# Optimization experiments

Hardware: AMD Instinct MI355X
Metric: run time of the kernel (lower is better)

The kernel has to match this reference:

```python
import jax, jax.numpy as jnp
import numpy as np

HID = 128  # args['hidden_size']


def preprocess_adj(A):
    # A: [B, N, N] -> D^{-1/2} (A + I) D^{-1/2}
    N = A.shape[1]
    A_hat = A + jnp.eye(N, dtype=A.dtype)
    d = jnp.sum(A_hat, axis=2)                     # [B, N]
    d_safe = jnp.where(d > 0, d, 1.0)
    d_inv = jnp.where(d > 0, d_safe ** -0.5, 0.0)  # inf -> 0, as in torch code
    return d_inv[:, :, None] * A_hat * d_inv[:, None, :]


def lstm(x, w_ih, w_hh, b_ih, b_hh):
    # x: [B, T, H]; PyTorch gate order i, f, g, o; zero init state
    B = x.shape[0]
    H = w_hh.shape[1]
    def step(carry, xt):
        h, c = carry
        z = xt @ w_ih.T + b_ih + h @ w_hh.T + b_hh
        i, f, g, o = jnp.split(z, 4, axis=-1)
        c = jax.nn.sigmoid(f) * c + jax.nn.sigmoid(i) * jnp.tanh(g)
        h = jax.nn.sigmoid(o) * jnp.tanh(c)
        return (h, c), h
    h0 = jnp.zeros((B, H), x.dtype)
    c0 = jnp.zeros((B, H), x.dtype)
    _, hs = jax.lax.scan(step, (h0, c0), jnp.swapaxes(x, 0, 1))
    return jnp.swapaxes(hs, 0, 1)  # [B, T, H]


def gcn_dynamic_forward(x, A_norm, conv_w, conv_b, w_ih, w_hh, b_ih, b_hh):
    # x: [B, N, HID] with N >= HID: take last HID rows as dynamic-filter input
    df_in = x[:, x.shape[1] - HID:, :]              # [B, HID, HID]
    dyn = jax.lax.conv_general_dilated(
        df_in, conv_w, window_strides=(1,), padding=[(1, 1)],
        dimension_numbers=('NCH', 'OIH', 'NCH')) + conv_b[None, :, None]
    lw = lstm(dyn, w_ih, w_hh, b_ih, b_hh)          # [B, HID, HID]
    agg = jnp.matmul(A_norm, x)                     # [B, N, HID]
    out = jax.nn.sigmoid(jnp.matmul(agg, lw))       # output activation (1-layer GCN)
    return out                                       # dropout is identity in eval


def setup_inputs() -> dict:
    key = jax.random.key(0)
    ks = jax.random.split(key, 8)
    B, N = 4, 4096
    node_embedding = jax.random.normal(ks[0], (B, N, HID), dtype=jnp.float32)
    # sparse symmetric-ish 0/1 adjacency, avg degree ~ N*0.01
    adjacency_matrix = (jax.random.uniform(ks[1], (B, N, N)) < 0.01).astype(jnp.float32)
    s = 0.05
    conv_w = jax.random.normal(ks[2], (HID, HID, 3), dtype=jnp.float32) * s
    conv_b = jax.random.normal(ks[3], (HID,), dtype=jnp.float32) * s
    w_ih = jax.random.normal(ks[4], (4 * HID, HID), dtype=jnp.float32) * s
    w_hh = jax.random.normal(ks[5], (4 * HID, HID), dtype=jnp.float32) * s
    b_ih = jax.random.normal(ks[6], (4 * HID,), dtype=jnp.float32) * s
    b_hh = jax.random.normal(ks[7], (4 * HID,), dtype=jnp.float32) * s
    return {"node_embedding": node_embedding, "adjacency_matrix": adjacency_matrix,
            "conv_w": conv_w, "conv_b": conv_b,
            "w_ih": w_ih, "w_hh": w_hh, "b_ih": b_ih, "b_hh": b_hh}


def reference(node_embedding, adjacency_matrix, conv_w, conv_b, w_ih, w_hh, b_ih, b_hh):
    A_norm = preprocess_adj(adjacency_matrix)
    return gcn_dynamic_forward(node_embedding, A_norm, conv_w, conv_b, w_ih, w_hh, b_ih, b_hh)
```

## Files before the change

### kernel.cpp

```cpp
#include <hip/hip_runtime.h>
#include <math.h>

#define N_NODES 4096
#define HIDN 128
#define MAXNZ 128

typedef float v4f __attribute__((ext_vector_type(4)));
typedef _Float16 h2 __attribute__((ext_vector_type(2)));
typedef _Float16 h8 __attribute__((ext_vector_type(8)));

__device__ __forceinline__ float fsig(float x) { return 1.0f / (1.0f + __expf(-x)); }
__device__ __forceinline__ float ftanh_(float x) { return 1.0f - 2.0f / (__expf(2.0f * x) + 1.0f); }

__global__ __launch_bounds__(512) void k1_conv_ascan(
        const float* __restrict__ x, const float* __restrict__ conv_w,
        const float* __restrict__ conv_b, const float* __restrict__ w_ih,
        const float* __restrict__ b_ih, const float* __restrict__ b_hh,
        float* __restrict__ z3,
        const float* __restrict__ A, float* __restrict__ d_inv,
        int* __restrict__ cnt, int* __restrict__ idx) {
    __shared__ __align__(16) float dyn_lds[4][HIDN];
    __shared__ int sidx[8][MAXNZ];
    if (blockIdx.x < 128) {
        const int cb = blockIdx.x;
        const int b = cb >> 5;
        const int t0 = (cb & 31) * 4;
        const int tsub = threadIdx.x >> 7;
        const int h = threadIdx.x & 127;
        const int t = t0 + tsub;
        {
            const float* xb = x + ((size_t)b * N_NODES + (N_NODES - HIDN)) * HIDN;
            const float* w = conv_w + (size_t)t * HIDN * 3;
            float a0 = conv_b[t], a1 = 0.0f, a2 = 0.0f, a3 = 0.0f;
            #pragma unroll 4
            for (int i = 0; i < HIDN; i += 4) {
                const float* xr0 = xb + (size_t)i * HIDN;
                #pragma unroll
                for (int s = 0; s < 4; ++s) {
                    const float* xr = xr0 + s * HIDN;
                    float w0 = w[(i + s) * 3 + 0], w1 = w[(i + s) * 3 + 1], w2 = w[(i + s) * 3 + 2];
                    float left  = (h > 0)   ? xr[h - 1] : 0.0f;
                    float mid   = xr[h];
                    float right = (h < 127) ? xr[h + 1] : 0.0f;
                    if (s == 0)      a0 += left * w0 + mid * w1 + right * w2;
                    else if (s == 1) a1 += left * w0 + mid * w1 + right * w2;
                    else if (s == 2) a2 += left * w0 + mid * w1 + right * w2;
                    else             a3 += left * w0 + mid * w1 + right * w2;
                }
            }
            dyn_lds[tsub][h] = (a0 + a1) + (a2 + a3);
        }
        __syncthreads();
        const int u = threadIdx.x;
        const int qg = u >> 7;
        const int m  = u & 127;
        const float4* wr = (const float4*)(w_ih + (size_t)u * HIDN);
        float bias = b_ih[u] + b_hh[u];
        float acc0 = bias, acc1 = bias, acc2 = bias, acc3 = bias;
        #pragma unroll
        for (int half = 0; half < 2; ++half) {
            float4 wv[16];
            #pragma unroll
            for (int j = 0; j < 16; ++j) wv[j] = wr[half * 16 + j];
            const float4* d0 = (const float4*)dyn_lds[0] + half * 16;
            const float4* d1 = (const float4*)dyn_lds[1] + half * 16;
            const float4* d2 = (const float4*)dyn_lds[2] + half * 16;
            const float4* d3 = (const float4*)dyn_lds[3] + half * 16;
            #pragma unroll
            for (int j = 0; j < 16; ++j) {
                float4 wj = wv[j];
                float4 v0 = d0[j], v1 = d1[j], v2 = d2[j], v3 = d3[j];
                acc0 += wj.x * v0.x + wj.y * v0.y + wj.z * v0.z + wj.w * v0.w;
                acc1 += wj.x * v1.x + wj.y * v1.y + wj.z * v1.z + wj.w * v1.w;
                acc2 += wj.x * v2.x + wj.y * v2.y + wj.z * v2.z + wj.w * v2.w;
                acc3 += wj.x * v3.x + wj.y * v3.y + wj.z * v3.z + wj.w * v3.w;
            }
        }
        float* zb = z3 + (size_t)b * HIDN * HIDN * 4;
        zb[((size_t)(t0 + 0) * 128 + m) * 4 + qg] = acc0;
        zb[((size_t)(t0 + 1) * 128 + m) * 4 + qg] = acc1;
        zb[((size_t)(t0 + 2) * 128 + m) * 4 + qg] = acc2;
        zb[((size_t)(t0 + 3) * 128 + m) * 4 + qg] = acc3;
    } else {
        const int wid = threadIdx.x >> 6;
        const int lane = threadIdx.x & 63;
        const int r = (blockIdx.x - 128) * 8 + wid;
        const v4f* row = (const v4f*)(A + (size_t)r * N_NODES);
        const unsigned long long below = (1ull << lane) - 1ull;
        int cbase = 0;
        v4f cur[4], nxt[4];
        #pragma unroll
        for (int j = 0; j < 4; ++j) cur[j] = row[j * 64 + lane];
#define PROC1(c, col)                                                         \
        {                                                                     \
            bool nz = ((c) != 0.0f);                                          \
            unsigned long long mm = __ballot(nz);                             \
            if (mm) {                                                         \
                if (nz) {                                                     \
                    int p_ = cbase + __popcll(mm & below);                    \
                    if (p_ < MAXNZ) sidx[wid][p_] = (col);                    \
                }                                                             \
                cbase += __popcll(mm);                                        \
            }                                                                 \
        }
        #pragma unroll
        for (int g = 0; g < 4; ++g) {
            if (g < 3) {
                #pragma unroll
                for (int j = 0; j < 4; ++j) nxt[j] = row[(g + 1) * 256 + j * 64 + lane];
            }
            #pragma unroll
            for (int j = 0; j < 4; ++j) {
                int col0 = ((g * 4 + j) * 64 + lane) * 4;
                PROC1(cur[j].x, col0 + 0);
                PROC1(cur[j].y, col0 + 1);
                PROC1(cur[j].z, col0 + 2);
                PROC1(cur[j].w, col0 + 3);
            }
            #pragma unroll
            for (int j = 0; j < 4; ++j) cur[j] = nxt[j];
        }
#undef PROC1
        int cnt_r = (cbase < MAXNZ) ? cbase : MAXNZ;
        for (int k = lane; k < cnt_r; k += 64)
            idx[r * MAXNZ + k] = sidx[wid][k];
        if (lane == 0) {
            cnt[r] = cnt_r;
            d_inv[r] = rsqrtf((float)(cbase + 1));
        }
    }
}

__global__ __launch_bounds__(512, 2) void k2_lstm_gather(
        const float* __restrict__ z3, const float* __restrict__ w_hh,
        float* __restrict__ lw,
        const float* __restrict__ x, const float* __restrict__ d_inv,
        const int* __restrict__ cnt, const int* __restrict__ idx,
        float* __restrict__ agg) {
    __shared__ __align__(16) float4 zl[16 * 128];
    __shared__ __align__(16) _Float16 hbuf[2][HIDN];
    if (blockIdx.x < 4) {
        const int b = blockIdx.x;
        const int t = threadIdx.x;
        const int m = t >> 2;
        const int q = t & 3;
        h2 w2[4][16];
        #pragma unroll
        for (int g = 0; g < 4; ++g) {
            const float4* wr = (const float4*)(w_hh + ((size_t)(g * HIDN + m)) * HIDN + q * 32);
            #pragma unroll
            for (int j4 = 0; j4 < 8; ++j4) {
                float4 wv = wr[j4];
                w2[g][2 * j4 + 0] = h2{(_Float16)wv.x, (_Float16)wv.y};
                w2[g][2 * j4 + 1] = h2{(_Float16)wv.z, (_Float16)wv.w};
            }
        }
        float c = 0.0f;
        if (t < 64) ((h2*)hbuf[0])[t] = h2{(_Float16)0.0f, (_Float16)0.0f};
        const float4* zsrc = (const float4*)z3 + (size_t)b * 16384;
        float* lwb = lw + (size_t)b * HIDN * HIDN + m;
        float hist[4];
        for (int ch = 0; ch < 8; ++ch) {
            const float4* src = zsrc + ch * 2048;
            #pragma unroll
            for (int k = 0; k < 4; ++k)
                zl[t + 512 * k] = src[t + 512 * k];
            __syncthreads();
            #pragma unroll
            for (int si = 0; si < 16; ++si) {
                const int s = ch * 16 + si;
                const h8* hp = ((const h8*)hbuf[s & 1]) + q * 4;
                h8 H0 = hp[0], H1 = hp[1], H2 = hp[2], H3 = hp[3];
                h2 hh[16];
                #pragma unroll
                for (int j = 0; j < 4; ++j) {
                    hh[j]      = ((const h2*)&H0)[j];
                    hh[4 + j]  = ((const h2*)&H1)[j];
                    hh[8 + j]  = ((const h2*)&H2)[j];
                    hh[12 + j] = ((const h2*)&H3)[j];
                }
                float4 zv = zl[si * 128 + m];
                float a0 = 0.f, a1 = 0.f, a2 = 0.f, a3 = 0.f;
                #pragma unroll
                for (int j = 0; j < 16; ++j) {
                    a0 = __builtin_amdgcn_fdot2(w2[0][j], hh[j], a0, false);
                    a1 = __builtin_amdgcn_fdot2(w2[1][j], hh[j], a1, false);
                    a2 = __builtin_amdgcn_fdot2(w2[2][j], hh[j], a2, false);
                    a3 = __builtin_amdgcn_fdot2(w2[3][j], hh[j], a3, false);
                }
                a0 += __shfl_xor(a0, 1); a0 += __shfl_xor(a0, 2);
                a1 += __shfl_xor(a1, 1); a1 += __shfl_xor(a1, 2);
                a2 += __shfl_xor(a2, 1); a2 += __shfl_xor(a2, 2);
                a3 += __shfl_xor(a3, 1); a3 += __shfl_xor(a3, 2);
                float zi = a0 + zv.x;
                float zf = a1 + zv.y;
                float zg = a2 + zv.z;
                float zo = a3 + zv.w;
                float ig = fsig(zi);
                float fg = fsig(zf);
                float gg = ftanh_(zg);
                float og = fsig(zo);
                c = fg * c + ig * gg;
                float hn = og * ftanh_(c);
                if (q == (si & 3)) hist[si >> 2] = hn;
                if (q == 0) hbuf[(s + 1) & 1][m] = (_Float16)hn;
                __syncthreads();
            }
            #pragma unroll
            for (int j = 0; j < 4; ++j)
                lwb[(size_t)(ch * 16 + q + 4 * j) * HIDN] = hist[j];
        }
    } else {
        const int gIdx = blockIdx.x - 4;
        const int b = (gIdx & 7) >> 1;
        const int o = ((gIdx >> 3) << 1) | (gIdx & 1);
        const int wid = threadIdx.x >> 6;
        const int lane = threadIdx.x & 63;
        float* dl = (float*)zl;
        {
            const float4* dsrc = (const float4*)(d_inv + (b << 12));
            float4* ddst = (float4*)dl;
            ddst[threadIdx.x] = dsrc[threadIdx.x];
            ddst[threadIdx.x + 512] = dsrc[threadIdx.x + 512];
        }
        __syncthreads();
        const int i = o * 8 + wid;
        const int r = (b << 12) + i;
        const float2* xb = (const float2*)(x + (size_t)b * N_NODES * HIDN);
        const int* irow = idx + r * MAXNZ;
        const int n = cnt[r];
        float ax = 0.0f, ay = 0.0f;
        int k = 0;
        for (; k + 8 <= n; k += 8) {
            int4 j0 = *(const int4*)&irow[k];
            int4 j1 = *(const int4*)&irow[k + 4];
            float2 v0 = xb[(size_t)j0.x * 64 + lane];
            float2 v1 = xb[(size_t)j0.y * 64 + lane];
            float2 v2 = xb[(size_t)j0.z * 64 + lane];
            float2 v3 = xb[(size_t)j0.w * 64 + lane];
            float2 v4 = xb[(size_t)j1.x * 64 + lane];
            float2 v5 = xb[(size_t)j1.y * 64 + lane];
            float2 v6 = xb[(size_t)j1.z * 64 + lane];
            float2 v7 = xb[(size_t)j1.w * 64 + lane];
            float d0 = dl[j0.x], d1 = dl[j0.y], d2 = dl[j0.z], d3 = dl[j0.w];
            float d4 = dl[j1.x], d5 = dl[j1.y], d6 = dl[j1.z], d7 = dl[j1.w];
            ax += d0 * v0.x + d1 * v1.x + d2 * v2.x + d3 * v3.x
                + d4 * v4.x + d5 * v5.x + d6 * v6.x + d7 * v7.x;
            ay += d0 * v0.y + d1 * v1.y + d2 * v2.y + d3 * v3.y
                + d4 * v4.y + d5 * v5.y + d6 * v6.y + d7 * v7.y;
        }
        for (; k < n; ++k) {
            int j = irow[k];
            float dj = dl[j];
            float2 v = xb[(size_t)j * 64 + lane];
            ax += dj * v.x;
            ay += dj * v.y;
        }
        float di = dl[i];
        float2 vi = xb[(size_t)i * 64 + lane];
        float2 o2;
        o2.x = di * (ax + di * vi.x);
        o2.y = di * (ay + di * vi.y);
        ((float2*)(agg + (size_t)r * HIDN))[lane] = o2;
    }
}

__global__ __launch_bounds__(256) void k_outmm(
        const float* __restrict__ agg, const float* __restrict__ lw,
        float* __restrict__ out) {
    __shared__ __align__(16) float lw_lds[HIDN * HIDN];
    const int i0 = blockIdx.x * 64;
    const int b = i0 >> 12;
    const float4* lwg = (const float4*)(lw + (size_t)b * HIDN * HIDN);
    float4* lds4 = (float4*)lw_lds;
    for (int v = threadIdx.x; v < HIDN * HIDN / 4; v += 256) lds4[v] = lwg[v];
    __syncthreads();
    const int r0 = i0 + (threadIdx.x >> 3) * 2;
    const int u0 = (threadIdx.x & 7) * 16;
    const float4* a4 = (const float4*)agg;
    float4 acc[2][4];
    #pragma unroll
    for (int rr = 0; rr < 2; ++rr)
        #pragma unroll
        for (int cc = 0; cc < 4; ++cc) acc[rr][cc] = make_float4(0.f, 0.f, 0.f, 0.f);
    for (int f4 = 0; f4 < 32; ++f4) {
        float4 a0 = a4[(size_t)r0 * 32 + f4];
        float4 a1 = a4[(size_t)(r0 + 1) * 32 + f4];
        #pragma unroll
        for (int ff = 0; ff < 4; ++ff) {
            float af0 = (ff == 0) ? a0.x : (ff == 1) ? a0.y : (ff == 2) ? a0.z : a0.w;
            float af1 = (ff == 0) ? a1.x : (ff == 1) ? a1.y : (ff == 2) ? a1.z : a1.w;
            int f = f4 * 4 + ff;
            const float4* wrow = (const float4*)(lw_lds + f * HIDN + u0);
            #pragma unroll
            for (int cc = 0; cc < 4; ++cc) {
                float4 wv = wrow[cc];
                acc[0][cc].x += af0 * wv.x; acc[0][cc].y += af0 * wv.y;
                acc[0][cc].z += af0 * wv.z; acc[0][cc].w += af0 * wv.w;
                acc[1][cc].x += af1 * wv.x; acc[1][cc].y += af1 * wv.y;
                acc[1][cc].z += af1 * wv.z; acc[1][cc].w += af1 * wv.w;
            }
        }
    }
    #pragma unroll
    for (int rr = 0; rr < 2; ++rr) {
        #pragma unroll
        for (int cc = 0; cc < 4; ++cc) {
            float4 ov;
            ov.x = fsig(acc[rr][cc].x);
            ov.y = fsig(acc[rr][cc].y);
            ov.z = fsig(acc[rr][cc].z);
            ov.w = fsig(acc[rr][cc].w);
            *(float4*)(out + (size_t)(r0 + rr) * HIDN + u0 + cc * 4) = ov;
        }
    }
}

extern "C" void kernel_launch(void* const* d_in, const int* in_sizes, int n_in,
                              void* d_out, int out_size, void* d_ws, size_t ws_size,
                              hipStream_t stream) {
    const float* x      = (const float*)d_in[0];
    const float* A      = (const float*)d_in[1];
    const float* conv_w = (const float*)d_in[2];
    const float* conv_b = (const float*)d_in[3];
    const float* w_ih   = (const float*)d_in[4];
    const float* w_hh   = (const float*)d_in[5];
    const float* b_ih   = (const float*)d_in[6];
    const float* b_hh   = (const float*)d_in[7];
    float* out = (float*)d_out;

    char* ws = (char*)d_ws;
    float* d_inv = (float*)ws;
    int*   cnt   = (int*)(ws + 65536);
    int*   idx   = (int*)(ws + 131072);
    float* z3    = (float*)(ws + 131072 + 8388608);
    float* lw    = (float*)(ws + 131072 + 8388608 + 1048576);
    float* agg   = (float*)(ws + 131072 + 8388608 + 1048576 + 262144);

    hipLaunchKernelGGL(k1_conv_ascan, dim3(2176), dim3(512), 0, stream,
                       x, conv_w, conv_b, w_ih, b_ih, b_hh, z3, A, d_inv, cnt, idx);
    hipLaunchKernelGGL(k2_lstm_gather, dim3(2052), dim3(512), 0, stream,
                       z3, w_hh, lw, x, d_inv, cnt, idx, agg);
    hipLaunchKernelGGL(k_outmm, dim3(256), dim3(256), 0, stream, agg, lw, out);
}
```

Before: 500.7 us.

## Overlap LSTM recurrence with adjacency scan and split gather into own kernel

Moves the adjacency-row scan from the conv kernel into the LSTM kernel so the serial 4-block LSTM recurrence runs alongside the memory-bound A scan rather than alongside the gather. The conv/z kernel and the gather now run as separate launches, giving four kernels in total. The output matmul is retiled to 512 threads over 32 rows per block with one row per thread. The LSTM inner loop also selects h pairs inline instead of staging them in an array. The extra launch and changed overlap could lengthen the critical path if the LSTM is the long pole.

```diff
diff --git a/kernel.cpp b/kernel.cpp
--- a/kernel.cpp
+++ b/kernel.cpp
@@ -12,133 +12,81 @@
 __device__ __forceinline__ float fsig(float x) { return 1.0f / (1.0f + __expf(-x)); }
 __device__ __forceinline__ float ftanh_(float x) { return 1.0f - 2.0f / (__expf(2.0f * x) + 1.0f); }
 
-__global__ __launch_bounds__(512) void k1_conv_ascan(
+__global__ __launch_bounds__(512) void k_convz(
         const float* __restrict__ x, const float* __restrict__ conv_w,
         const float* __restrict__ conv_b, const float* __restrict__ w_ih,
         const float* __restrict__ b_ih, const float* __restrict__ b_hh,
-        float* __restrict__ z3,
+        float* __restrict__ z3) {
+    const int cb = blockIdx.x;
+    const int b = cb >> 5;
+    const int t0 = (cb & 31) * 4;
+    const int tsub = threadIdx.x >> 7;
+    const int h = threadIdx.x & 127;
+    const int t = t0 + tsub;
+    __shared__ __align__(16) float dyn_lds[4][HIDN];
+    {
+        const float* xb = x + ((size_t)b * N_NODES + (N_NODES - HIDN)) * HIDN;
+        const float* w = conv_w + (size_t)t * HIDN * 3;
+        float a0 = conv_b[t], a1 = 0.0f, a2 = 0.0f, a3 = 0.0f;
+        #pragma unroll 4
+        for (int i = 0; i < HIDN; i += 4) {
+            const float* xr0 = xb + (size_t)i * HIDN;
+            #pragma unroll
+            for (int s = 0; s < 4; ++s) {
+                const float* xr = xr0 + s * HIDN;
+                float w0 = w[(i + s) * 3 + 0], w1 = w[(i + s) * 3 + 1], w2 = w[(i + s) * 3 + 2];
+                float left  = (h > 0)   ? xr[h - 1] : 0.0f;
+                float mid   = xr[h];
+                float right = (h < 127) ? xr[h + 1] : 0.0f;
+                if (s == 0)      a0 += left * w0 + mid * w1 + right * w2;
+                else if (s == 1) a1 += left * w0 + mid * w1 + right * w2;
+                else if (s == 2) a2 += left * w0 + mid * w1 + right * w2;
+                else             a3 += left * w0 + mid * w1 + right * w2;
+            }
+        }
+        dyn_lds[tsub][h] = (a0 + a1) + (a2 + a3);
+    }
+    __syncthreads();
+    const int u = threadIdx.x;
+    const int qg = u >> 7;
+    const int m  = u & 127;
+    const float4* wr = (const float4*)(w_ih + (size_t)u * HIDN);
+    float bias = b_ih[u] + b_hh[u];
+    float acc0 = bias, acc1 = bias, acc2 = bias, acc3 = bias;
+    #pragma unroll
+    for (int half = 0; half < 2; ++half) {
+        float4 wv[16];
+        #pragma unroll
+        for (int j = 0; j < 16; ++j) wv[j] = wr[half * 16 + j];
+        const float4* d0 = (const float4*)dyn_lds[0] + half * 16;
+        const float4* d1 = (const float4*)dyn_lds[1] + half * 16;
+        const float4* d2 = (const float4*)dyn_lds[2] + half * 16;
+        const float4* d3 = (const float4*)dyn_lds[3] + half * 16;
+        #pragma unroll
+        for (int j = 0; j < 16; ++j) {
+            float4 wj = wv[j];
+            float4 v0 = d0[j], v1 = d1[j], v2 = d2[j], v3 = d3[j];
+            acc0 += wj.x * v0.x + wj.y * v0.y + wj.z * v0.z + wj.w * v0.w;
+            acc1 += wj.x * v1.x + wj.y * v1.y + wj.z * v1.z + wj.w * v1.w;
+            acc2 += wj.x * v2.x + wj.y * v2.y + wj.z * v2.z + wj.w * v2.w;
+            acc3 += wj.x * v3.x + wj.y * v3.y + wj.z * v3.z + wj.w * v3.w;
+        }
+    }
+    float* zb = z3 + (size_t)b * HIDN * HIDN * 4;
+    zb[((size_t)(t0 + 0) * 128 + m) * 4 + qg] = acc0;
+    zb[((size_t)(t0 + 1) * 128 + m) * 4 + qg] = acc1;
+    zb[((size_t)(t0 + 2) * 128 + m) * 4 + qg] = acc2;
+    zb[((size_t)(t0 + 3) * 128 + m) * 4 + qg] = acc3;
+}
+
+__global__ __launch_bounds__(512, 2) void k_lstm_scan(
+        const float* __restrict__ z3, const float* __restrict__ w_hh,
+        float* __restrict__ lw,
         const float* __restrict__ A, float* __restrict__ d_inv,
         int* __restrict__ cnt, int* __restrict__ idx) {
-    __shared__ __align__(16) float dyn_lds[4][HIDN];
-    __shared__ int sidx[8][MAXNZ];
-    if (blockIdx.x < 128) {
-        const int cb = blockIdx.x;
-        const int b = cb >> 5;
-        const int t0 = (cb & 31) * 4;
-        const int tsub = threadIdx.x >> 7;
-        const int h = threadIdx.x & 127;
-        const int t = t0 + tsub;
-        {
-            const float* xb = x + ((size_t)b * N_NODES + (N_NODES - HIDN)) * HIDN;
-            const float* w = conv_w + (size_t)t * HIDN * 3;
-            float a0 = conv_b[t], a1 = 0.0f, a2 = 0.0f, a3 = 0.0f;
-            #pragma unroll 4
-            for (int i = 0; i < HIDN; i += 4) {
-                const float* xr0 = xb + (size_t)i * HIDN;
-                #pragma unroll
-                for (int s = 0; s < 4; ++s) {
-                    const float* xr = xr0 + s * HIDN;
-                    float w0 = w[(i + s) * 3 + 0], w1 = w[(i + s) * 3 + 1], w2 = w[(i + s) * 3 + 2];
-                    float left  = (h > 0)   ? xr[h - 1] : 0.0f;
-                    float mid   = xr[h];
-                    float right = (h < 127) ? xr[h + 1] : 0.0f;
-                    if (s == 0)      a0 += left * w0 + mid * w1 + right * w2;
-                    else if (s == 1) a1 += left * w0 + mid * w1 + right * w2;
-                    else if (s == 2) a2 += left * w0 + mid * w1 + right * w2;
-                    else             a3 += left * w0 + mid * w1 + right * w2;
-                }
-            }
-            dyn_lds[tsub][h] = (a0 + a1) + (a2 + a3);
-        }
-        __syncthreads();
-        const int u = threadIdx.x;
-        const int qg = u >> 7;
-        const int m  = u & 127;
-        const float4* wr = (const float4*)(w_ih + (size_t)u * HIDN);
-        float bias = b_ih[u] + b_hh[u];
-        float acc0 = bias, acc1 = bias, acc2 = bias, acc3 = bias;
-        #pragma unroll
-        for (int half = 0; half < 2; ++half) {
-            float4 wv[16];
-            #pragma unroll
-            for (int j = 0; j < 16; ++j) wv[j] = wr[half * 16 + j];
-            const float4* d0 = (const float4*)dyn_lds[0] + half * 16;
-            const float4* d1 = (const float4*)dyn_lds[1] + half * 16;
-            const float4* d2 = (const float4*)dyn_lds[2] + half * 16;
-            const float4* d3 = (const float4*)dyn_lds[3] + half * 16;
-            #pragma unroll
-            for (int j = 0; j < 16; ++j) {
-                float4 wj = wv[j];
-                float4 v0 = d0[j], v1 = d1[j], v2 = d2[j], v3 = d3[j];
-                acc0 += wj.x * v0.x + wj.y * v0.y + wj.z * v0.z + wj.w * v0.w;
-                acc1 += wj.x * v1.x + wj.y * v1.y + wj.z * v1.z + wj.w * v1.w;
-                acc2 += wj.x * v2.x + wj.y * v2.y + wj.z * v2.z + wj.w * v2.w;
-                acc3 += wj.x * v3.x + wj.y * v3.y + wj.z * v3.z + wj.w * v3.w;
-            }
-        }
-        float* zb = z3 + (size_t)b * HIDN * HIDN * 4;
-        zb[((size_t)(t0 + 0) * 128 + m) * 4 + qg] = acc0;
-        zb[((size_t)(t0 + 1) * 128 + m) * 4 + qg] = acc1;
-        zb[((size_t)(t0 + 2) * 128 + m) * 4 + qg] = acc2;
-        zb[((size_t)(t0 + 3) * 128 + m) * 4 + qg] = acc3;
-    } else {
-        const int wid = threadIdx.x >> 6;
-        const int lane = threadIdx.x & 63;
-        const int r = (blockIdx.x - 128) * 8 + wid;
-        const v4f* row = (const v4f*)(A + (size_t)r * N_NODES);
-        const unsigned long long below = (1ull << lane) - 1ull;
-        int cbase = 0;
-        v4f cur[4], nxt[4];
-        #pragma unroll
-        for (int j = 0; j < 4; ++j) cur[j] = row[j * 64 + lane];
-#define PROC1(c, col)                                                         \
-        {                                                                     \
-            bool nz = ((c) != 0.0f);                                          \
-            unsigned long long mm = __ballot(nz);                             \
-            if (mm) {                                                         \
-                if (nz) {                                                     \
-                    int p_ = cbase + __popcll(mm & below);                    \
-                    if (p_ < MAXNZ) sidx[wid][p_] = (col);                    \
-                }                                                             \
-                cbase += __popcll(mm);                                        \
-            }                                                                 \
-        }
-        #pragma unroll
-        for (int g = 0; g < 4; ++g) {
-            if (g < 3) {
-                #pragma unroll
-                for (int j = 0; j < 4; ++j) nxt[j] = row[(g + 1) * 256 + j * 64 + lane];
-            }
-            #pragma unroll
-            for (int j = 0; j < 4; ++j) {
-                int col0 = ((g * 4 + j) * 64 + lane) * 4;
-                PROC1(cur[j].x, col0 + 0);
-                PROC1(cur[j].y, col0 + 1);
-                PROC1(cur[j].z, col0 + 2);
-                PROC1(cur[j].w, col0 + 3);
-            }
-            #pragma unroll
-            for (int j = 0; j < 4; ++j) cur[j] = nxt[j];
-        }
-#undef PROC1
-        int cnt_r = (cbase < MAXNZ) ? cbase : MAXNZ;
-        for (int k = lane; k < cnt_r; k += 64)
-            idx[r * MAXNZ + k] = sidx[wid][k];
-        if (lane == 0) {
-            cnt[r] = cnt_r;
-            d_inv[r] = rsqrtf((float)(cbase + 1));
-        }
-    }
-}
-
-__global__ __launch_bounds__(512, 2) void k2_lstm_gather(
-        const float* __restrict__ z3, const float* __restrict__ w_hh,
-        float* __restrict__ lw,
-        const float* __restrict__ x, const float* __restrict__ d_inv,
-        const int* __restrict__ cnt, const int* __restrict__ idx,
-        float* __restrict__ agg) {
     __shared__ __align__(16) float4 zl[16 * 128];
     __shared__ __align__(16) _Float16 hbuf[2][HIDN];
+    __shared__ int sidx[8][MAXNZ];
     if (blockIdx.x < 4) {
         const int b = blockIdx.x;
         const int t = threadIdx.x;
@@ -171,22 +119,18 @@
                 const int s = ch * 16 + si;
                 const h8* hp = ((const h8*)hbuf[s & 1]) + q * 4;
                 h8 H0 = hp[0], H1 = hp[1], H2 = hp[2], H3 = hp[3];
-                h2 hh[16];
-                #pragma unroll
-                for (int j = 0; j < 4; ++j) {
-                    hh[j]      = ((const h2*)&H0)[j];
-                    hh[4 + j]  = ((const h2*)&H1)[j];
-                    hh[8 + j]  = ((const h2*)&H2)[j];
-                    hh[12 + j] = ((const h2*)&H3)[j];
-                }
                 float4 zv = zl[si * 128 + m];
                 float a0 = 0.f, a1 = 0.f, a2 = 0.f, a3 = 0.f;
                 #pragma unroll
                 for (int j = 0; j < 16; ++j) {
-                    a0 = __builtin_amdgcn_fdot2(w2[0][j], hh[j], a0, false);
-                    a1 = __builtin_amdgcn_fdot2(w2[1][j], hh[j], a1, false);
-                    a2 = __builtin_amdgcn_fdot2(w2[2][j], hh[j], a2, false);
-                    a3 = __builtin_amdgcn_fdot2(w2[3][j], hh[j], a3, false);
+                    h2 hj = (j < 4)  ? ((const h2*)&H0)[j]
+                          : (j < 8)  ? ((const h2*)&H1)[j - 4]
+                          : (j < 12) ? ((const h2*)&H2)[j - 8]
+                                     : ((const h2*)&H3)[j - 12];
+                    a0 = __builtin_amdgcn_fdot2(w2[0][j], hj, a0, false);
+                    a1 = __builtin_amdgcn_fdot2(w2[1][j], hj, a1, false);
+                    a2 = __builtin_amdgcn_fdot2(w2[2][j], hj, a2, false);
+                    a3 = __builtin_amdgcn_fdot2(w2[3][j], hj, a3, false);
                 }
                 a0 += __shfl_xor(a0, 1); a0 += __shfl_xor(a0, 2);
                 a1 += __shfl_xor(a1, 1); a1 += __shfl_xor(a1, 2);
@@ -211,108 +155,150 @@
                 lwb[(size_t)(ch * 16 + q + 4 * j) * HIDN] = hist[j];
         }
     } else {
-        const int gIdx = blockIdx.x - 4;
-        const int b = (gIdx & 7) >> 1;
-        const int o = ((gIdx >> 3) << 1) | (gIdx & 1);
         const int wid = threadIdx.x >> 6;
         const int lane = threadIdx.x & 63;
-        float* dl = (float*)zl;
-        {
-            const float4* dsrc = (const float4*)(d_inv + (b << 12));
-            float4* ddst = (float4*)dl;
-            ddst[threadIdx.x] = dsrc[threadIdx.x];
-            ddst[threadIdx.x + 512] = dsrc[threadIdx.x + 512];
-        }
-        __syncthreads();
-        const int i = o * 8 + wid;
-        const int r = (b << 12) + i;
-        const float2* xb = (const float2*)(x + (size_t)b * N_NODES * HIDN);
-        const int* irow = idx + r * MAXNZ;
-        const int n = cnt[r];
-        float ax = 0.0f, ay = 0.0f;
-        int k = 0;
-        for (; k + 8 <= n; k += 8) {
-            int4 j0 = *(const int4*)&irow[k];
-            int4 j1 = *(const int4*)&irow[k + 4];
-            float2 v0 = xb[(size_t)j0.x * 64 + lane];
-            float2 v1 = xb[(size_t)j0.y * 64 + lane];
-            float2 v2 = xb[(size_t)j0.z * 64 + lane];
-            float2 v3 = xb[(size_t)j0.w * 64 + lane];
-            float2 v4 = xb[(size_t)j1.x * 64 + lane];
-            float2 v5 = xb[(size_t)j1.y * 64 + lane];
-            float2 v6 = xb[(size_t)j1.z * 64 + lane];
-            float2 v7 = xb[(size_t)j1.w * 64 + lane];
-            float d0 = dl[j0.x], d1 = dl[j0.y], d2 = dl[j0.z], d3 = dl[j0.w];
-            float d4 = dl[j1.x], d5 = dl[j1.y], d6 = dl[j1.z], d7 = dl[j1.w];
-            ax += d0 * v0.x + d1 * v1.x + d2 * v2.x + d3 * v3.x
-                + d4 * v4.x + d5 * v5.x + d6 * v6.x + d7 * v7.x;
-            ay += d0 * v0.y + d1 * v1.y + d2 * v2.y + d3 * v3.y
-                + d4 * v4.y + d5 * v5.y + d6 * v6.y + d7 * v7.y;
-        }
-        for (; k < n; ++k) {
-            int j = irow[k];
-            float dj = dl[j];
-            float2 v = xb[(size_t)j * 64 + lane];
-            ax += dj * v.x;
-            ay += dj * v.y;
-        }
-        float di = dl[i];
-        float2 vi = xb[(size_t)i * 64 + lane];
-        float2 o2;
-        o2.x = di * (ax + di * vi.x);
-        o2.y = di * (ay + di * vi.y);
-        ((float2*)(agg + (size_t)r * HIDN))[lane] = o2;
-    }
-}
-
-__global__ __launch_bounds__(256) void k_outmm(
+        const int r = (blockIdx.x - 4) * 8 + wid;
+        const v4f* row = (const v4f*)(A + (size_t)r * N_NODES);
+        const unsigned long long below = (1ull << lane) - 1ull;
+        int cbase = 0;
+        v4f cur[4], nxt[4];
+        #pragma unroll
+        for (int j = 0; j < 4; ++j) cur[j] = row[j * 64 + lane];
+#define PROC1(c, col)                                                         \
+        {                                                                     \
+            bool nz = ((c) != 0.0f);                                          \
+            unsigned long long mm = __ballot(nz);                             \
+            if (mm) {                                                         \
+                if (nz) {                                                     \
+                    int p_ = cbase + __popcll(mm & below);                    \
+                    if (p_ < MAXNZ) sidx[wid][p_] = (col);                    \
+                }                                                             \
+                cbase += __popcll(mm);                                        \
+            }                                                                 \
+        }
+        #pragma unroll
+        for (int g = 0; g < 4; ++g) {
+            if (g < 3) {
+                #pragma unroll
+                for (int j = 0; j < 4; ++j) nxt[j] = row[(g + 1) * 256 + j * 64 + lane];
+            }
+            #pragma unroll
+            for (int j = 0; j < 4; ++j) {
+                int col0 = ((g * 4 + j) * 64 + lane) * 4;
+                PROC1(cur[j].x, col0 + 0);
+                PROC1(cur[j].y, col0 + 1);
+                PROC1(cur[j].z, col0 + 2);
+                PROC1(cur[j].w, col0 + 3);
+            }
+            #pragma unroll
+            for (int j = 0; j < 4; ++j) cur[j] = nxt[j];
+        }
+#undef PROC1
+        int cnt_r = (cbase < MAXNZ) ? cbase : MAXNZ;
+        for (int k = lane; k < cnt_r; k += 64)
+            idx[r * MAXNZ + k] = sidx[wid][k];
+        if (lane == 0) {
+            cnt[r] = cnt_r;
+            d_inv[r] = rsqrtf((float)(cbase + 1));
+        }
+    }
+}
+
+__global__ __launch_bounds__(512) void k_gather(
+        const float* __restrict__ x, const float* __restrict__ d_inv,
+        const int* __restrict__ cnt, const int* __restrict__ idx,
+        float* __restrict__ agg) {
+    const int gIdx = blockIdx.x;
+    const int b = (gIdx & 7) >> 1;
+    const int o = ((gIdx >> 3) << 1) | (gIdx & 1);
+    const int wid = threadIdx.x >> 6;
+    const int lane = threadIdx.x & 63;
+    __shared__ __align__(16) float dl[N_NODES];
+    {
+        const float4* dsrc = (const float4*)(d_inv + (b << 12));
+        float4* ddst = (float4*)dl;
+        ddst[threadIdx.x] = dsrc[threadIdx.x];
+        ddst[threadIdx.x + 512] = dsrc[threadIdx.x + 512];
+    }
+    __syncthreads();
+    const int i = o * 8 + wid;
+    const int r = (b << 12) + i;
+    const float2* xb = (const float2*)(x + (size_t)b * N_NODES * HIDN);
+    const int* irow = idx + r * MAXNZ;
+    const int n = cnt[r];
+    float ax = 0.0f, ay = 0.0f;
+    int k = 0;
+    for (; k + 8 <= n; k += 8) {
+        int4 j0 = *(const int4*)&irow[k];
+        int4 j1 = *(const int4*)&irow[k + 4];
+        float2 v0 = xb[(size_t)j0.x * 64 + lane];
+        float2 v1 = xb[(size_t)j0.y * 64 + lane];
+        float2 v2 = xb[(size_t)j0.z * 64 + lane];
+        float2 v3 = xb[(size_t)j0.w * 64 + lane];
+        float2 v4 = xb[(size_t)j1.x * 64 + lane];
+        float2 v5 = xb[(size_t)j1.y * 64 + lane];
+        float2 v6 = xb[(size_t)j1.z * 64 + lane];
+        float2 v7 = xb[(size_t)j1.w * 64 + lane];
+        float d0 = dl[j0.x], d1 = dl[j0.y], d2 = dl[j0.z], d3 = dl[j0.w];
+        float d4 = dl[j1.x], d5 = dl[j1.y], d6 = dl[j1.z], d7 = dl[j1.w];
+        ax += d0 * v0.x + d1 * v1.x + d2 * v2.x + d3 * v3.x
+            + d4 * v4.x + d5 * v5.x + d6 * v6.x + d7 * v7.x;
+        ay += d0 * v0.y + d1 * v1.y + d2 * v2.y + d3 * v3.y
+            + d4 * v4.y + d5 * v5.y + d6 * v6.y + d7 * v7.y;
+    }
+    for (; k < n; ++k) {
+        int j = irow[k];
+        float dj = dl[j];
+        float2 v = xb[(size_t)j * 64 + lane];
+        ax += dj * v.x;
+        ay += dj * v.y;
+    }
+    float di = dl[i];
+    float2 vi = xb[(size_t)i * 64 + lane];
+    float2 o2;
+    o2.x = di * (ax + di * vi.x);
+    o2.y = di * (ay + di * vi.y);
+    ((float2*)(agg + (size_t)r * HIDN))[lane] = o2;
+}
+
+__global__ __launch_bounds__(512) void k_outmm(
         const float* __restrict__ agg, const float* __restrict__ lw,
         float* __restrict__ out) {
     __shared__ __align__(16) float lw_lds[HIDN * HIDN];
-    const int i0 = blockIdx.x * 64;
+    const int i0 = blockIdx.x * 32;
     const int b = i0 >> 12;
     const float4* lwg = (const float4*)(lw + (size_t)b * HIDN * HIDN);
     float4* lds4 = (float4*)lw_lds;
-    for (int v = threadIdx.x; v < HIDN * HIDN / 4; v += 256) lds4[v] = lwg[v];
+    for (int v = threadIdx.x; v < HIDN * HIDN / 4; v += 512) lds4[v] = lwg[v];
     __syncthreads();
-    const int r0 = i0 + (threadIdx.x >> 3) * 2;
-    const int u0 = (threadIdx.x & 7) * 16;
+    const int r0 = i0 + (threadIdx.x >> 4);
+    const int u0 = (threadIdx.x & 15) * 4;
     const float4* a4 = (const float4*)agg;
-    float4 acc[2][4];
-    #pragma unroll
-    for (int rr = 0; rr < 2; ++rr)
-        #pragma unroll
-        for (int cc = 0; cc < 4; ++cc) acc[rr][cc] = make_float4(0.f, 0.f, 0.f, 0.f);
+    float4 acc[2];
+    acc[0] = make_float4(0.f, 0.f, 0.f, 0.f);
+    acc[1] = make_float4(0.f, 0.f, 0.f, 0.f);
     for (int f4 = 0; f4 < 32; ++f4) {
         float4 a0 = a4[(size_t)r0 * 32 + f4];
-        float4 a1 = a4[(size_t)(r0 + 1) * 32 + f4];
         #pragma unroll
         for (int ff = 0; ff < 4; ++ff) {
             float af0 = (ff == 0) ? a0.x : (ff == 1) ? a0.y : (ff == 2) ? a0.z : a0.w;
-            float af1 = (ff == 0) ? a1.x : (ff == 1) ? a1.y : (ff == 2) ? a1.z : a1.w;
-            int f = f4 * 4 + ff;
-            const float4* wrow = (const float4*)(lw_lds + f * HIDN + u0);
-            #pragma unroll
-            for (int cc = 0; cc < 4; ++cc) {
-                float4 wv = wrow[cc];
-                acc[0][cc].x += af0 * wv.x; acc[0][cc].y += af0 * wv.y;
-                acc[0][cc].z += af0 * wv.z; acc[0][cc].w += af0 * wv.w;
-                acc[1][cc].x += af1 * wv.x; acc[1][cc].y += af1 * wv.y;
-                acc[1][cc].z += af1 * wv.z; acc[1][cc].w += af1 * wv.w;
+            const float* wrow = lw_lds + (f4 * 4 + ff) * HIDN + u0;
+            #pragma unroll
+            for (int cc = 0; cc < 2; ++cc) {
+                float4 wv = *(const float4*)(wrow + cc * 64);
+                acc[cc].x += af0 * wv.x; acc[cc].y += af0 * wv.y;
+                acc[cc].z += af0 * wv.z; acc[cc].w += af0 * wv.w;
             }
         }
     }
     #pragma unroll
-    for (int rr = 0; rr < 2; ++rr) {
-        #pragma unroll
-        for (int cc = 0; cc < 4; ++cc) {
-            float4 ov;
-            ov.x = fsig(acc[rr][cc].x);
-            ov.y = fsig(acc[rr][cc].y);
-            ov.z = fsig(acc[rr][cc].z);
-            ov.w = fsig(acc[rr][cc].w);
-            *(float4*)(out + (size_t)(r0 + rr) * HIDN + u0 + cc * 4) = ov;
-        }
+    for (int cc = 0; cc < 2; ++cc) {
+        float4 ov;
+        ov.x = fsig(acc[cc].x);
+        ov.y = fsig(acc[cc].y);
+        ov.z = fsig(acc[cc].z);
+        ov.w = fsig(acc[cc].w);
+        *(float4*)(out + (size_t)r0 * HIDN + u0 + cc * 64) = ov;
     }
 }
 
@@ -337,9 +323,11 @@
     float* lw    = (float*)(ws + 131072 + 8388608 + 1048576);
     float* agg   = (float*)(ws + 131072 + 8388608 + 1048576 + 262144);
 
-    hipLaunchKernelGGL(k1_conv_ascan, dim3(2176), dim3(512), 0, stream,
-                       x, conv_w, conv_b, w_ih, b_ih, b_hh, z3, A, d_inv, cnt, idx);
-    hipLaunchKernelGGL(k2_lstm_gather, dim3(2052), dim3(512), 0, stream,
-                       z3, w_hh, lw, x, d_inv, cnt, idx, agg);
-    hipLaunchKernelGGL(k_outmm, dim3(256), dim3(256), 0, stream, agg, lw, out);
-}
+    hipLaunchKernelGGL(k_convz, dim3(128), dim3(512), 0, stream,
+                       x, conv_w, conv_b, w_ih, b_ih, b_hh, z3);
+    hipLaunchKernelGGL(k_lstm_scan, dim3(2052), dim3(512), 0, stream,
+                       z3, w_hh, lw, A, d_inv, cnt, idx);
+    hipLaunchKernelGGL(k_gather, dim3(2048), dim3(512), 0, stream,
+                       x, d_inv, cnt, idx, agg);
+    hipLaunchKernelGGL(k_outmm, dim3(512), dim3(512), 0, stream, agg, lw, out);
+}
```

After: 507.4 us. Within noise of the previous version (+1.3%).
